# Performance work log

Measured on AMD Instinct MI355X. Metric: run time of the kernel, lower is better.

Reference implementation:

```python
import jax, jax.numpy as jnp
import numpy as np

EPS = 1e-06

def phi(x):
    # canonical linear-attention feature map: elu(x) + 1 (positive features)
    return jax.nn.elu(x) + 1.0

def setup_inputs() -> dict:
    key = jax.random.key(0)
    kq, kk, kv = jax.random.split(key, 3)
    B, H, S, D = 4, 16, 4096, 64
    query = jax.random.normal(kq, (B, H, S, D), dtype=jnp.float32)
    k = jax.random.normal(kk, (B, H, S, D), dtype=jnp.float32)
    value = jax.random.normal(kv, (B, H, S, D), dtype=jnp.float32)
    attention_mask = jnp.ones((B, S), dtype=jnp.float32)
    return {"query": query, "key": k, "value": value, "attention_mask": attention_mask}

def reference(query, key, value, attention_mask):
    B, H, S, D = query.shape
    q = query / jnp.sqrt(jnp.asarray(D, query.dtype))
    phi_q = phi(q)                                   # [b,h,n,d]
    phi_k = phi(key)                                 # [b,h,n,d]
    mask = attention_mask[:, None, :, None].astype(phi_k.dtype)  # [b,1,n,1]
    phi_k = phi_k * mask
    kv_term = jnp.einsum('bhnd,bhnv->bhdv', phi_k, value)        # [b,h,d,v]
    output = jnp.einsum('bhnd,bhdv->bhnv', phi_q, kv_term)       # [b,h,n,v]
    k_one = jnp.sum(phi_k, axis=2)                               # [b,h,d] == phi_k @ masked ones
    normalizer = jnp.einsum('bhnd,bhd->bhn', phi_q, k_one)[..., None]  # [b,h,n,1]
    return output / (normalizer + EPS)
```

## Files before the change

### kernel.cpp

```cpp
#include <hip/hip_runtime.h>

#define NB 4
#define NH 16
#define NS 4096
#define ND 64
#define NBH (NB * NH)
#define EPSF 1e-6f

#define P1_CHUNKS 16
#define P1_ROWS (NS / P1_CHUNKS)
#define P2_ROWS 128

__device__ __forceinline__ float phi_f(float x) {
    return x > 0.0f ? x + 1.0f : __expf(x);
}

template<bool PART>
__global__ __launch_bounds__(256, 2)
void la_pass1(const float* __restrict__ Kin, const float* __restrict__ Vin,
              const float* __restrict__ Min, float* __restrict__ okv,
              float* __restrict__ ok1)
{
    const int t  = threadIdx.x;
    const int cx = blockIdx.x;
    const int bh = blockIdx.y;
    const int bb = bh >> 4;
    const long long base = (long long)bh * NS * ND;
    const float* Kb = Kin + base;
    const float* Vb = Vin + base;
    const float* Mb = Min + (long long)bb * NS;

    __shared__ float sk[64 * ND];
    __shared__ float sv[64 * ND];

    const int lrow = t >> 4;
    const int lcol = (t & 15) * 4;
    const int d0 = (t >> 4) * 4;
    const int v0 = (t & 15) * 4;

    float acc[4][4] = {};
    float k1p[4] = {0.f, 0.f, 0.f, 0.f};

    const int s0 = cx * P1_ROWS;

    float4 kr[4], vr[4];
    float  mr[4];
    #pragma unroll
    for (int i = 0; i < 4; ++i) {
        const int r = lrow + 16 * i;
        const long long g = (long long)(s0 + r) * ND + lcol;
        kr[i] = *(const float4*)(Kb + g);
        vr[i] = *(const float4*)(Vb + g);
        mr[i] = Mb[s0 + r];
    }

    for (int tile = 0; tile < P1_ROWS; tile += 64) {
        __syncthreads();
        #pragma unroll
        for (int i = 0; i < 4; ++i) {
            const int r = lrow + 16 * i;
            float4 pk;
            pk.x = phi_f(kr[i].x) * mr[i];
            pk.y = phi_f(kr[i].y) * mr[i];
            pk.z = phi_f(kr[i].z) * mr[i];
            pk.w = phi_f(kr[i].w) * mr[i];
            k1p[0] += pk.x; k1p[1] += pk.y;
            k1p[2] += pk.z; k1p[3] += pk.w;
            *(float4*)(sk + r * ND + lcol) = pk;
            *(float4*)(sv + r * ND + lcol) = vr[i];
        }
        if (tile + 64 < P1_ROWS) {
            const int nb = s0 + tile + 64;
            #pragma unroll
            for (int i = 0; i < 4; ++i) {
                const int r = lrow + 16 * i;
                const long long g = (long long)(nb + r) * ND + lcol;
                kr[i] = *(const float4*)(Kb + g);
                vr[i] = *(const float4*)(Vb + g);
                mr[i] = Mb[nb + r];
            }
        }
        __syncthreads();
        #pragma unroll 4
        for (int r = 0; r < 64; ++r) {
            const float4 a = *(const float4*)(sk + r * ND + d0);
            const float4 b = *(const float4*)(sv + r * ND + v0);
            const float av[4] = {a.x, a.y, a.z, a.w};
            const float bv[4] = {b.x, b.y, b.z, b.w};
            #pragma unroll
            for (int i = 0; i < 4; ++i)
                #pragma unroll
                for (int j = 0; j < 4; ++j)
                    acc[i][j] += av[i] * bv[j];
        }
    }

    __syncthreads();
    #pragma unroll
    for (int i = 0; i < 4; ++i)
        #pragma unroll
        for (int j = 0; j < 4; ++j)
            sk[(d0 + i) * ND + v0 + j] = acc[i][j];
    #pragma unroll
    for (int c = 0; c < 4; ++c)
        sv[lrow * ND + lcol + c] = k1p[c];
    __syncthreads();

    if (PART) {
        float* pkv = okv + (long long)(bh * P1_CHUNKS + cx) * (ND * ND);
        #pragma unroll
        for (int i = 0; i < 4; ++i)
            ((float4*)pkv)[t + 256 * i] = ((const float4*)sk)[t + 256 * i];
        if (t < ND) {
            float s = 0.f;
            #pragma unroll
            for (int g = 0; g < 16; ++g) s += sv[g * ND + t];
            ok1[(bh * P1_CHUNKS + cx) * ND + t] = s;
        }
    } else {
        float* kvb = okv + (long long)bh * ND * ND;
        #pragma unroll
        for (int i = 0; i < 16; ++i)
            atomicAdd(&kvb[t + 256 * i], sk[t + 256 * i]);
        if (t < ND) {
            float s = 0.f;
            #pragma unroll
            for (int g = 0; g < 16; ++g) s += sv[g * ND + t];
            atomicAdd(&ok1[bh * ND + t], s);
        }
    }
}

__global__ __launch_bounds__(256)
void la_reduce(const float* __restrict__ pkv, const float* __restrict__ pk1,
               float* __restrict__ kv, float* __restrict__ k1)
{
    const int t = threadIdx.x;
    const int bh = blockIdx.x;
    const float4* src = (const float4*)(pkv + (long long)bh * P1_CHUNKS * ND * ND);
    float4 a[4];
    #pragma unroll
    for (int i = 0; i < 4; ++i) { a[i].x = 0.f; a[i].y = 0.f; a[i].z = 0.f; a[i].w = 0.f; }
    for (int c = 0; c < P1_CHUNKS; ++c) {
        #pragma unroll
        for (int i = 0; i < 4; ++i) {
            const float4 v = src[c * 1024 + t + 256 * i];
            a[i].x += v.x; a[i].y += v.y; a[i].z += v.z; a[i].w += v.w;
        }
    }
    float4* dst = (float4*)(kv + (long long)bh * ND * ND);
    #pragma unroll
    for (int i = 0; i < 4; ++i) dst[t + 256 * i] = a[i];
    if (t < ND) {
        float s = 0.f;
        for (int c = 0; c < P1_CHUNKS; ++c) s += pk1[(bh * P1_CHUNKS + c) * ND + t];
        k1[bh * ND + t] = s;
    }
}

__global__ __launch_bounds__(256, 2)
void la_pass2(const float* __restrict__ Qin, const float* __restrict__ KV,
              const float* __restrict__ K1, float* __restrict__ Out)
{
    const int t  = threadIdx.x;
    const int bh = blockIdx.y;
    const int s0 = blockIdx.x * P2_ROWS;
    const long long base = (long long)bh * NS * ND;

    __shared__ float skv[ND * ND];
    __shared__ float sq[P2_ROWS * 65];
    __shared__ float sk1[ND];

    {
        const float4* src = (const float4*)(KV + (long long)bh * ND * ND);
        #pragma unroll
        for (int i = 0; i < 4; ++i) ((float4*)skv)[t + 256 * i] = src[t + 256 * i];
        if (t < 16) ((float4*)sk1)[t] = ((const float4*)(K1 + bh * ND))[t];
    }
    {
        const int lrow = t >> 4;
        const int lcol = (t & 15) * 4;
        #pragma unroll
        for (int hb = 0; hb < 2; ++hb) {
            float4 q4[4];
            #pragma unroll
            for (int i = 0; i < 4; ++i) {
                const int r = lrow + 16 * (4 * hb + i);
                q4[i] = *(const float4*)(Qin + base + (long long)(s0 + r) * ND + lcol);
            }
            #pragma unroll
            for (int i = 0; i < 4; ++i) {
                const int r = lrow + 16 * (4 * hb + i);
                sq[r * 65 + lcol + 0] = phi_f(q4[i].x * 0.125f);
                sq[r * 65 + lcol + 1] = phi_f(q4[i].y * 0.125f);
                sq[r * 65 + lcol + 2] = phi_f(q4[i].z * 0.125f);
                sq[r * 65 + lcol + 3] = phi_f(q4[i].w * 0.125f);
            }
        }
    }
    __syncthreads();

    const int r0 = (t >> 3) * 4;
    const int v0 = (t & 7) * 8;

    float acc[4][8] = {};
    float nacc[4] = {0.f, 0.f, 0.f, 0.f};

    #pragma unroll 4
    for (int d = 0; d < ND; ++d) {
        const float s1 = sk1[d];
        float q[4];
        #pragma unroll
        for (int j = 0; j < 4; ++j) q[j] = sq[(r0 + j) * 65 + d];
        const float4 b0 = *(const float4*)(skv + d * ND + v0);
        const float4 b1 = *(const float4*)(skv + d * ND + v0 + 4);
        const float bv[8] = {b0.x, b0.y, b0.z, b0.w, b1.x, b1.y, b1.z, b1.w};
        #pragma unroll
        for (int j = 0; j < 4; ++j) {
            nacc[j] += q[j] * s1;
            #pragma unroll
            for (int k = 0; k < 8; ++k)
                acc[j][k] += q[j] * bv[k];
        }
    }

    float* outb = Out + base;
    #pragma unroll
    for (int j = 0; j < 4; ++j) {
        const float rn = 1.0f / (nacc[j] + EPSF);
        float4 o0, o1;
        o0.x = acc[j][0] * rn; o0.y = acc[j][1] * rn;
        o0.z = acc[j][2] * rn; o0.w = acc[j][3] * rn;
        o1.x = acc[j][4] * rn; o1.y = acc[j][5] * rn;
        o1.z = acc[j][6] * rn; o1.w = acc[j][7] * rn;
        *(float4*)(outb + (long long)(s0 + r0 + j) * ND + v0)     = o0;
        *(float4*)(outb + (long long)(s0 + r0 + j) * ND + v0 + 4) = o1;
    }
}

extern "C" void kernel_launch(void* const* d_in, const int* in_sizes, int n_in,
                              void* d_out, int out_size, void* d_ws, size_t ws_size,
                              hipStream_t stream)
{
    const float* Q = (const float*)d_in[0];
    const float* K = (const float*)d_in[1];
    const float* V = (const float*)d_in[2];
    const float* M = (const float*)d_in[3];
    float* Out = (float*)d_out;

    const size_t partf = (size_t)NBH * P1_CHUNKS * ND * ND;
    const size_t pk1f  = (size_t)NBH * P1_CHUNKS * ND;
    const size_t kvf   = (size_t)NBH * ND * ND;
    const size_t k1f   = (size_t)NBH * ND;
    const size_t need  = (partf + pk1f + kvf + k1f) * sizeof(float);

    if (ws_size >= need) {
        float* PKV = (float*)d_ws;
        float* PK1 = PKV + partf;
        float* KVb = PK1 + pk1f;
        float* K1b = KVb + kvf;
        la_pass1<true><<<dim3(P1_CHUNKS, NBH), dim3(256), 0, stream>>>(K, V, M, PKV, PK1);
        la_reduce<<<dim3(NBH), dim3(256), 0, stream>>>(PKV, PK1, KVb, K1b);
        la_pass2<<<dim3(NS / P2_ROWS, NBH), dim3(256), 0, stream>>>(Q, KVb, K1b, Out);
    } else {
        float* KVb = (float*)d_ws;
        float* K1b = KVb + kvf;
        hipMemsetAsync(d_ws, 0, (kvf + k1f) * sizeof(float), stream);
        la_pass1<false><<<dim3(P1_CHUNKS, NBH), dim3(256), 0, stream>>>(K, V, M, KVb, K1b);
        la_pass2<<<dim3(NS / P2_ROWS, NBH), dim3(256), 0, stream>>>(Q, KVb, K1b, Out);
    }
}
```

Baseline: 263.9 us.

## Use bf16x3 split MFMA for both KV accumulation and output passes

Replaces the scalar FMA loops in both passes with MFMA 16x16x32 bf16 instructions. Each fp32 operand is split into high and low bf16 parts and three products are summed to approximate fp32 accuracy. Pass2 folds the normalizer into an extra padded column block of the B matrix, so the k1 dot product comes out of the same MFMA; it is then broadcast with a shuffle. The register prefetch double-buffering in pass1 is dropped, and the split conversion adds ALU work and shared-memory traffic, which risks exposing load latency.

```diff
diff --git a/kernel.cpp b/kernel.cpp
--- a/kernel.cpp
+++ b/kernel.cpp
@@ -1,22 +1,49 @@
 #include <hip/hip_runtime.h>
+
+typedef unsigned short ushort_t;
+typedef unsigned int uint32;
+typedef __bf16 bf16x8 __attribute__((ext_vector_type(8)));
+typedef float f32x4 __attribute__((ext_vector_type(4)));
 
 #define NB 4
 #define NH 16
 #define NS 4096
 #define ND 64
-#define NBH (NB * NH)
+#define NBH 64
 #define EPSF 1e-6f
 
-#define P1_CHUNKS 16
-#define P1_ROWS (NS / P1_CHUNKS)
-#define P2_ROWS 128
+#define CH1 16
+#define ROWS1 (NS / CH1)
+#define P2R 128
+#define LDJ 70
+#define LDJW 35
 
 __device__ __forceinline__ float phi_f(float x) {
     return x > 0.0f ? x + 1.0f : __expf(x);
 }
+__device__ __forceinline__ ushort_t bf16_rn(float x) {
+    uint32 u = __float_as_uint(x);
+    uint32 r = (u + 0x7FFFu + ((u >> 16) & 1u)) >> 16;
+    return (ushort_t)r;
+}
+__device__ __forceinline__ void split2(float x, ushort_t& h, ushort_t& l) {
+    h = bf16_rn(x);
+    float hf = __uint_as_float(((uint32)h) << 16);
+    l = bf16_rn(x - hf);
+}
+union FragU { uint32 u[4]; bf16x8 v; };
+__device__ __forceinline__ bf16x8 ld_frag(const ushort_t* arr, int widx) {
+    const uint32* p = (const uint32*)arr;
+    FragU f;
+    f.u[0] = p[widx]; f.u[1] = p[widx + 1]; f.u[2] = p[widx + 2]; f.u[3] = p[widx + 3];
+    return f.v;
+}
+__device__ __forceinline__ f32x4 mfma16(bf16x8 a, bf16x8 b, f32x4 c) {
+    return __builtin_amdgcn_mfma_f32_16x16x32_bf16(a, b, c, 0, 0, 0);
+}
 
 template<bool PART>
-__global__ __launch_bounds__(256, 2)
+__global__ __launch_bounds__(256)
 void la_pass1(const float* __restrict__ Kin, const float* __restrict__ Vin,
               const float* __restrict__ Min, float* __restrict__ okv,
               float* __restrict__ ok1)
@@ -25,109 +52,119 @@
     const int cx = blockIdx.x;
     const int bh = blockIdx.y;
     const int bb = bh >> 4;
-    const long long base = (long long)bh * NS * ND;
-    const float* Kb = Kin + base;
-    const float* Vb = Vin + base;
+    const float* Kb = Kin + (long long)bh * NS * ND;
+    const float* Vb = Vin + (long long)bh * NS * ND;
     const float* Mb = Min + (long long)bb * NS;
 
-    __shared__ float sk[64 * ND];
-    __shared__ float sv[64 * ND];
-
-    const int lrow = t >> 4;
-    const int lcol = (t & 15) * 4;
-    const int d0 = (t >> 4) * 4;
-    const int v0 = (t & 15) * 4;
-
-    float acc[4][4] = {};
-    float k1p[4] = {0.f, 0.f, 0.f, 0.f};
-
-    const int s0 = cx * P1_ROWS;
-
-    float4 kr[4], vr[4];
-    float  mr[4];
-    #pragma unroll
-    for (int i = 0; i < 4; ++i) {
-        const int r = lrow + 16 * i;
-        const long long g = (long long)(s0 + r) * ND + lcol;
-        kr[i] = *(const float4*)(Kb + g);
-        vr[i] = *(const float4*)(Vb + g);
-        mr[i] = Mb[s0 + r];
-    }
-
-    for (int tile = 0; tile < P1_ROWS; tile += 64) {
+    __shared__ __align__(16) ushort_t skh[64 * LDJ], skl[64 * LDJ];
+    __shared__ __align__(16) ushort_t svh[64 * LDJ], svl[64 * LDJ];
+
+    const int p  = t & 31;
+    const int c0 = (t >> 5) * 8;
+    const int wv = t >> 6;
+    const int m  = t & 15;
+    const int q  = (t & 63) >> 4;
+    const int lane = t & 63;
+
+    const f32x4 zf = {0.f, 0.f, 0.f, 0.f};
+    f32x4 acc0 = zf, acc1 = zf, acc2 = zf, acc3 = zf;
+    float k1loc[8] = {0.f,0.f,0.f,0.f,0.f,0.f,0.f,0.f};
+
+    const int s0 = cx * ROWS1;
+
+    for (int tile = 0; tile < ROWS1 / 64; ++tile) {
+        const int rb = s0 + tile * 64;
         __syncthreads();
+        {
+            const int r0 = rb + 2 * p;
+            const float4 ka = *(const float4*)(Kb + (long long)r0 * ND + c0);
+            const float4 kb2 = *(const float4*)(Kb + (long long)r0 * ND + c0 + 4);
+            const float4 kc = *(const float4*)(Kb + (long long)(r0 + 1) * ND + c0);
+            const float4 kd = *(const float4*)(Kb + (long long)(r0 + 1) * ND + c0 + 4);
+            const float4 va = *(const float4*)(Vb + (long long)r0 * ND + c0);
+            const float4 vb2 = *(const float4*)(Vb + (long long)r0 * ND + c0 + 4);
+            const float4 vc = *(const float4*)(Vb + (long long)(r0 + 1) * ND + c0);
+            const float4 vd = *(const float4*)(Vb + (long long)(r0 + 1) * ND + c0 + 4);
+            const float m0 = Mb[r0], m1 = Mb[r0 + 1];
+            const float kr0[8] = {ka.x,ka.y,ka.z,ka.w,kb2.x,kb2.y,kb2.z,kb2.w};
+            const float kr1[8] = {kc.x,kc.y,kc.z,kc.w,kd.x,kd.y,kd.z,kd.w};
+            const float vr0[8] = {va.x,va.y,va.z,va.w,vb2.x,vb2.y,vb2.z,vb2.w};
+            const float vr1[8] = {vc.x,vc.y,vc.z,vc.w,vd.x,vd.y,vd.z,vd.w};
+            #pragma unroll
+            for (int i = 0; i < 8; ++i) {
+                const float x0 = phi_f(kr0[i]) * m0;
+                const float x1 = phi_f(kr1[i]) * m1;
+                k1loc[i] += x0 + x1;
+                ushort_t h0, l0, h1, l1;
+                split2(x0, h0, l0); split2(x1, h1, l1);
+                const int widx = (c0 + i) * LDJW + p;
+                ((uint32*)skh)[widx] = (uint32)h0 | ((uint32)h1 << 16);
+                ((uint32*)skl)[widx] = (uint32)l0 | ((uint32)l1 << 16);
+                split2(vr0[i], h0, l0); split2(vr1[i], h1, l1);
+                ((uint32*)svh)[widx] = (uint32)h0 | ((uint32)h1 << 16);
+                ((uint32*)svl)[widx] = (uint32)l0 | ((uint32)l1 << 16);
+            }
+        }
+        __syncthreads();
+        #pragma unroll
+        for (int ks = 0; ks < 2; ++ks) {
+            const int fo = ks * 16 + q * 4;
+            const bf16x8 ah = ld_frag(skh, (16 * wv + m) * LDJW + fo);
+            const bf16x8 al = ld_frag(skl, (16 * wv + m) * LDJW + fo);
+            {
+                const bf16x8 fbh = ld_frag(svh, (0 + m) * LDJW + fo);
+                const bf16x8 fbl = ld_frag(svl, (0 + m) * LDJW + fo);
+                acc0 = mfma16(al, fbh, acc0); acc0 = mfma16(ah, fbl, acc0); acc0 = mfma16(ah, fbh, acc0);
+            }
+            {
+                const bf16x8 fbh = ld_frag(svh, (16 + m) * LDJW + fo);
+                const bf16x8 fbl = ld_frag(svl, (16 + m) * LDJW + fo);
+                acc1 = mfma16(al, fbh, acc1); acc1 = mfma16(ah, fbl, acc1); acc1 = mfma16(ah, fbh, acc1);
+            }
+            {
+                const bf16x8 fbh = ld_frag(svh, (32 + m) * LDJW + fo);
+                const bf16x8 fbl = ld_frag(svl, (32 + m) * LDJW + fo);
+                acc2 = mfma16(al, fbh, acc2); acc2 = mfma16(ah, fbl, acc2); acc2 = mfma16(ah, fbh, acc2);
+            }
+            {
+                const bf16x8 fbh = ld_frag(svh, (48 + m) * LDJW + fo);
+                const bf16x8 fbl = ld_frag(svl, (48 + m) * LDJW + fo);
+                acc3 = mfma16(al, fbh, acc3); acc3 = mfma16(ah, fbl, acc3); acc3 = mfma16(ah, fbh, acc3);
+            }
+        }
+    }
+
+    const int dbase = 16 * wv + q * 4;
+    if (PART) {
+        float* outp = okv + (long long)(bh * CH1 + cx) * (ND * ND);
         #pragma unroll
         for (int i = 0; i < 4; ++i) {
-            const int r = lrow + 16 * i;
-            float4 pk;
-            pk.x = phi_f(kr[i].x) * mr[i];
-            pk.y = phi_f(kr[i].y) * mr[i];
-            pk.z = phi_f(kr[i].z) * mr[i];
-            pk.w = phi_f(kr[i].w) * mr[i];
-            k1p[0] += pk.x; k1p[1] += pk.y;
-            k1p[2] += pk.z; k1p[3] += pk.w;
-            *(float4*)(sk + r * ND + lcol) = pk;
-            *(float4*)(sv + r * ND + lcol) = vr[i];
-        }
-        if (tile + 64 < P1_ROWS) {
-            const int nb = s0 + tile + 64;
-            #pragma unroll
-            for (int i = 0; i < 4; ++i) {
-                const int r = lrow + 16 * i;
-                const long long g = (long long)(nb + r) * ND + lcol;
-                kr[i] = *(const float4*)(Kb + g);
-                vr[i] = *(const float4*)(Vb + g);
-                mr[i] = Mb[nb + r];
-            }
-        }
-        __syncthreads();
-        #pragma unroll 4
-        for (int r = 0; r < 64; ++r) {
-            const float4 a = *(const float4*)(sk + r * ND + d0);
-            const float4 b = *(const float4*)(sv + r * ND + v0);
-            const float av[4] = {a.x, a.y, a.z, a.w};
-            const float bv[4] = {b.x, b.y, b.z, b.w};
-            #pragma unroll
-            for (int i = 0; i < 4; ++i)
-                #pragma unroll
-                for (int j = 0; j < 4; ++j)
-                    acc[i][j] += av[i] * bv[j];
-        }
-    }
-
+            outp[(dbase + i) * ND +  0 + m] = acc0[i];
+            outp[(dbase + i) * ND + 16 + m] = acc1[i];
+            outp[(dbase + i) * ND + 32 + m] = acc2[i];
+            outp[(dbase + i) * ND + 48 + m] = acc3[i];
+        }
+    } else {
+        float* outp = okv + (long long)bh * (ND * ND);
+        #pragma unroll
+        for (int i = 0; i < 4; ++i) {
+            atomicAdd(&outp[(dbase + i) * ND +  0 + m], acc0[i]);
+            atomicAdd(&outp[(dbase + i) * ND + 16 + m], acc1[i]);
+            atomicAdd(&outp[(dbase + i) * ND + 32 + m], acc2[i]);
+            atomicAdd(&outp[(dbase + i) * ND + 48 + m], acc3[i]);
+        }
+    }
     __syncthreads();
-    #pragma unroll
-    for (int i = 0; i < 4; ++i)
-        #pragma unroll
-        for (int j = 0; j < 4; ++j)
-            sk[(d0 + i) * ND + v0 + j] = acc[i][j];
-    #pragma unroll
-    for (int c = 0; c < 4; ++c)
-        sv[lrow * ND + lcol + c] = k1p[c];
+    float* red = (float*)skh;
+    #pragma unroll
+    for (int i = 0; i < 8; ++i) red[(c0 + i) * 33 + p] = k1loc[i];
     __syncthreads();
-
-    if (PART) {
-        float* pkv = okv + (long long)(bh * P1_CHUNKS + cx) * (ND * ND);
-        #pragma unroll
-        for (int i = 0; i < 4; ++i)
-            ((float4*)pkv)[t + 256 * i] = ((const float4*)sk)[t + 256 * i];
-        if (t < ND) {
-            float s = 0.f;
-            #pragma unroll
-            for (int g = 0; g < 16; ++g) s += sv[g * ND + t];
-            ok1[(bh * P1_CHUNKS + cx) * ND + t] = s;
-        }
-    } else {
-        float* kvb = okv + (long long)bh * ND * ND;
-        #pragma unroll
-        for (int i = 0; i < 16; ++i)
-            atomicAdd(&kvb[t + 256 * i], sk[t + 256 * i]);
-        if (t < ND) {
-            float s = 0.f;
-            #pragma unroll
-            for (int g = 0; g < 16; ++g) s += sv[g * ND + t];
-            atomicAdd(&ok1[bh * ND + t], s);
-        }
+    if (t < 64) {
+        float s = 0.f;
+        #pragma unroll
+        for (int pp = 0; pp < 32; ++pp) s += red[t * 33 + pp];
+        if (PART) ok1[(bh * CH1 + cx) * ND + t] = s;
+        else      atomicAdd(&ok1[bh * ND + t], s);
     }
 }
 
@@ -137,11 +174,11 @@
 {
     const int t = threadIdx.x;
     const int bh = blockIdx.x;
-    const float4* src = (const float4*)(pkv + (long long)bh * P1_CHUNKS * ND * ND);
+    const float4* src = (const float4*)(pkv + (long long)bh * CH1 * ND * ND);
     float4 a[4];
     #pragma unroll
     for (int i = 0; i < 4; ++i) { a[i].x = 0.f; a[i].y = 0.f; a[i].z = 0.f; a[i].w = 0.f; }
-    for (int c = 0; c < P1_CHUNKS; ++c) {
+    for (int c = 0; c < CH1; ++c) {
         #pragma unroll
         for (int i = 0; i < 4; ++i) {
             const float4 v = src[c * 1024 + t + 256 * i];
@@ -153,88 +190,115 @@
     for (int i = 0; i < 4; ++i) dst[t + 256 * i] = a[i];
     if (t < ND) {
         float s = 0.f;
-        for (int c = 0; c < P1_CHUNKS; ++c) s += pk1[(bh * P1_CHUNKS + c) * ND + t];
+        for (int c = 0; c < CH1; ++c) s += pk1[(bh * CH1 + c) * ND + t];
         k1[bh * ND + t] = s;
     }
 }
 
-__global__ __launch_bounds__(256, 2)
-void la_pass2(const float* __restrict__ Qin, const float* __restrict__ KV,
-              const float* __restrict__ K1, float* __restrict__ Out)
+__global__ __launch_bounds__(256)
+void la_pass2(const float* __restrict__ Qin, const float* __restrict__ KVin,
+              const float* __restrict__ K1in, float* __restrict__ Out)
 {
     const int t  = threadIdx.x;
     const int bh = blockIdx.y;
-    const int s0 = blockIdx.x * P2_ROWS;
+    const int s0 = blockIdx.x * P2R;
     const long long base = (long long)bh * NS * ND;
 
-    __shared__ float skv[ND * ND];
-    __shared__ float sq[P2_ROWS * 65];
-    __shared__ float sk1[ND];
+    __shared__ __align__(16) ushort_t sAh[P2R * LDJ], sAl[P2R * LDJ];
+    __shared__ __align__(16) ushort_t sBh[80 * LDJ],  sBl[80 * LDJ];
 
     {
-        const float4* src = (const float4*)(KV + (long long)bh * ND * ND);
-        #pragma unroll
-        for (int i = 0; i < 4; ++i) ((float4*)skv)[t + 256 * i] = src[t + 256 * i];
-        if (t < 16) ((float4*)sk1)[t] = ((const float4*)(K1 + bh * ND))[t];
-    }
-    {
-        const int lrow = t >> 4;
-        const int lcol = (t & 15) * 4;
-        #pragma unroll
-        for (int hb = 0; hb < 2; ++hb) {
-            float4 q4[4];
+        const float* KVb = KVin + (long long)bh * ND * ND;
+        const int d  = t >> 4;
+        const int v4 = (t & 15) * 4;
+        #pragma unroll
+        for (int it = 0; it < 4; ++it) {
+            const int dd = d + 16 * it;
+            const float4 kv = *(const float4*)(KVb + dd * ND + v4);
+            const float vals[4] = {kv.x, kv.y, kv.z, kv.w};
             #pragma unroll
             for (int i = 0; i < 4; ++i) {
-                const int r = lrow + 16 * (4 * hb + i);
-                q4[i] = *(const float4*)(Qin + base + (long long)(s0 + r) * ND + lcol);
-            }
+                ushort_t h, l; split2(vals[i], h, l);
+                sBh[(v4 + i) * LDJ + dd] = h;
+                sBl[(v4 + i) * LDJ + dd] = l;
+            }
+        }
+        if (t < 64) {
+            ushort_t h, l; split2(K1in[bh * ND + t], h, l);
+            sBh[64 * LDJ + t] = h; sBl[64 * LDJ + t] = l;
+        }
+        for (int z = t; z < 15 * 64; z += 256) {
+            const int n  = 65 + (z >> 6);
+            const int dd = z & 63;
+            sBh[n * LDJ + dd] = 0; sBl[n * LDJ + dd] = 0;
+        }
+    }
+    {
+        const int lr = t >> 4;
+        const int lc = (t & 15) * 4;
+        #pragma unroll
+        for (int it = 0; it < 8; ++it) {
+            const int r = lr + 16 * it;
+            const float4 q4 = *(const float4*)(Qin + base + (long long)(s0 + r) * ND + lc);
+            const float xs[4] = {q4.x, q4.y, q4.z, q4.w};
+            ushort_t h[4], l[4];
             #pragma unroll
-            for (int i = 0; i < 4; ++i) {
-                const int r = lrow + 16 * (4 * hb + i);
-                sq[r * 65 + lcol + 0] = phi_f(q4[i].x * 0.125f);
-                sq[r * 65 + lcol + 1] = phi_f(q4[i].y * 0.125f);
-                sq[r * 65 + lcol + 2] = phi_f(q4[i].z * 0.125f);
-                sq[r * 65 + lcol + 3] = phi_f(q4[i].w * 0.125f);
-            }
+            for (int i = 0; i < 4; ++i) split2(phi_f(xs[i] * 0.125f), h[i], l[i]);
+            const int w0 = (r * LDJ + lc) >> 1;
+            ((uint32*)sAh)[w0]     = (uint32)h[0] | ((uint32)h[1] << 16);
+            ((uint32*)sAh)[w0 + 1] = (uint32)h[2] | ((uint32)h[3] << 16);
+            ((uint32*)sAl)[w0]     = (uint32)l[0] | ((uint32)l[1] << 16);
+            ((uint32*)sAl)[w0 + 1] = (uint32)l[2] | ((uint32)l[3] << 16);
         }
     }
     __syncthreads();
 
-    const int r0 = (t >> 3) * 4;
-    const int v0 = (t & 7) * 8;
-
-    float acc[4][8] = {};
-    float nacc[4] = {0.f, 0.f, 0.f, 0.f};
-
-    #pragma unroll 4
-    for (int d = 0; d < ND; ++d) {
-        const float s1 = sk1[d];
-        float q[4];
-        #pragma unroll
-        for (int j = 0; j < 4; ++j) q[j] = sq[(r0 + j) * 65 + d];
-        const float4 b0 = *(const float4*)(skv + d * ND + v0);
-        const float4 b1 = *(const float4*)(skv + d * ND + v0 + 4);
-        const float bv[8] = {b0.x, b0.y, b0.z, b0.w, b1.x, b1.y, b1.z, b1.w};
-        #pragma unroll
-        for (int j = 0; j < 4; ++j) {
-            nacc[j] += q[j] * s1;
-            #pragma unroll
-            for (int k = 0; k < 8; ++k)
-                acc[j][k] += q[j] * bv[k];
+    const int wv = t >> 6;
+    const int m  = t & 15;
+    const int q  = (t & 63) >> 4;
+    const int lane = t & 63;
+
+    const f32x4 zf = {0.f, 0.f, 0.f, 0.f};
+    f32x4 acc[2][5];
+    #pragma unroll
+    for (int a = 0; a < 2; ++a)
+        #pragma unroll
+        for (int b = 0; b < 5; ++b) acc[a][b] = zf;
+
+    #pragma unroll
+    for (int ks = 0; ks < 2; ++ks) {
+        const int fo = ks * 16 + q * 4;
+        const bf16x8 a0h = ld_frag(sAh, (16 * (2 * wv + 0) + m) * LDJW + fo);
+        const bf16x8 a0l = ld_frag(sAl, (16 * (2 * wv + 0) + m) * LDJW + fo);
+        const bf16x8 a1h = ld_frag(sAh, (16 * (2 * wv + 1) + m) * LDJW + fo);
+        const bf16x8 a1l = ld_frag(sAl, (16 * (2 * wv + 1) + m) * LDJW + fo);
+        #pragma unroll
+        for (int nt = 0; nt < 5; ++nt) {
+            const bf16x8 fbh = ld_frag(sBh, (16 * nt + m) * LDJW + fo);
+            const bf16x8 fbl = ld_frag(sBl, (16 * nt + m) * LDJW + fo);
+            acc[0][nt] = mfma16(a0l, fbh, acc[0][nt]);
+            acc[0][nt] = mfma16(a0h, fbl, acc[0][nt]);
+            acc[0][nt] = mfma16(a0h, fbh, acc[0][nt]);
+            acc[1][nt] = mfma16(a1l, fbh, acc[1][nt]);
+            acc[1][nt] = mfma16(a1h, fbl, acc[1][nt]);
+            acc[1][nt] = mfma16(a1h, fbh, acc[1][nt]);
         }
     }
 
     float* outb = Out + base;
     #pragma unroll
-    for (int j = 0; j < 4; ++j) {
-        const float rn = 1.0f / (nacc[j] + EPSF);
-        float4 o0, o1;
-        o0.x = acc[j][0] * rn; o0.y = acc[j][1] * rn;
-        o0.z = acc[j][2] * rn; o0.w = acc[j][3] * rn;
-        o1.x = acc[j][4] * rn; o1.y = acc[j][5] * rn;
-        o1.z = acc[j][6] * rn; o1.w = acc[j][7] * rn;
-        *(float4*)(outb + (long long)(s0 + r0 + j) * ND + v0)     = o0;
-        *(float4*)(outb + (long long)(s0 + r0 + j) * ND + v0 + 4) = o1;
+    for (int mtl = 0; mtl < 2; ++mtl) {
+        const int rbase = s0 + 16 * (2 * wv + mtl) + q * 4;
+        #pragma unroll
+        for (int i = 0; i < 4; ++i) {
+            const float nv = __shfl(acc[mtl][4][i], lane & 48, 64);
+            const float rn = 1.0f / (nv + EPSF);
+            const long long ro = (long long)(rbase + i) * ND;
+            outb[ro +  0 + m] = acc[mtl][0][i] * rn;
+            outb[ro + 16 + m] = acc[mtl][1][i] * rn;
+            outb[ro + 32 + m] = acc[mtl][2][i] * rn;
+            outb[ro + 48 + m] = acc[mtl][3][i] * rn;
+        }
     }
 }
 
@@ -248,8 +312,8 @@
     const float* M = (const float*)d_in[3];
     float* Out = (float*)d_out;
 
-    const size_t partf = (size_t)NBH * P1_CHUNKS * ND * ND;
-    const size_t pk1f  = (size_t)NBH * P1_CHUNKS * ND;
+    const size_t partf = (size_t)NBH * CH1 * ND * ND;
+    const size_t pk1f  = (size_t)NBH * CH1 * ND;
     const size_t kvf   = (size_t)NBH * ND * ND;
     const size_t k1f   = (size_t)NBH * ND;
     const size_t need  = (partf + pk1f + kvf + k1f) * sizeof(float);
@@ -259,14 +323,14 @@
         float* PK1 = PKV + partf;
         float* KVb = PK1 + pk1f;
         float* K1b = KVb + kvf;
-        la_pass1<true><<<dim3(P1_CHUNKS, NBH), dim3(256), 0, stream>>>(K, V, M, PKV, PK1);
+        la_pass1<true><<<dim3(CH1, NBH), dim3(256), 0, stream>>>(K, V, M, PKV, PK1);
         la_reduce<<<dim3(NBH), dim3(256), 0, stream>>>(PKV, PK1, KVb, K1b);
-        la_pass2<<<dim3(NS / P2_ROWS, NBH), dim3(256), 0, stream>>>(Q, KVb, K1b, Out);
+        la_pass2<<<dim3(NS / P2R, NBH), dim3(256), 0, stream>>>(Q, KVb, K1b, Out);
     } else {
         float* KVb = (float*)d_ws;
         float* K1b = KVb + kvf;
         hipMemsetAsync(d_ws, 0, (kvf + k1f) * sizeof(float), stream);
-        la_pass1<false><<<dim3(P1_CHUNKS, NBH), dim3(256), 0, stream>>>(K, V, M, KVb, K1b);
-        la_pass2<<<dim3(NS / P2_ROWS, NBH), dim3(256), 0, stream>>>(Q, KVb, K1b, Out);
-    }
-}
+        la_pass1<false><<<dim3(CH1, NBH), dim3(256), 0, stream>>>(K, V, M, KVb, K1b);
+        la_pass2<<<dim3(NS / P2R, NBH), dim3(256), 0, stream>>>(Q, KVb, K1b, Out);
+    }
+}
```

After: 243.0 us. 1.09x faster.
